# Kernel tuning notes

Hardware: AMD Instinct MI355X
Metric: run time of the kernel (lower is better)

Reference implementation:

```python
import jax, jax.numpy as jnp
import numpy as np

N, E = 10000, 320000
IN_CH, HID, OUT_CH, HEADS = 128, 64, 40, 8
NEG_SLOPE = 0.2


def gat_conv(x, src, dst, W, a_src, a_dst, bias, heads, C, concat, n_nodes):
    # x: [N, F_in]; W: [F_in, heads*C]; a_src/a_dst: [heads, C]
    h = (x @ W).reshape(n_nodes, heads, C)              # [N,H,C]
    alpha_src = jnp.sum(h * a_src, axis=-1)             # [N,H]
    alpha_dst = jnp.sum(h * a_dst, axis=-1)             # [N,H]
    score = jax.nn.leaky_relu(alpha_src[src] + alpha_dst[dst], NEG_SLOPE)  # [E,H]
    # segment softmax over edges sharing the same destination node
    smax = jax.ops.segment_max(score, dst, num_segments=n_nodes)
    smax = jnp.where(jnp.isfinite(smax), smax, 0.0)
    ex = jnp.exp(score - smax[dst])
    denom = jax.ops.segment_sum(ex, dst, num_segments=n_nodes)
    alpha = ex / (denom[dst] + 1e-16)                   # [E,H]
    msg = h[src] * alpha[:, :, None]                    # [E,H,C]
    out = jax.ops.segment_sum(msg, dst, num_segments=n_nodes)  # [N,H,C]
    out = out.reshape(n_nodes, heads * C) if concat else out.mean(axis=1)
    return out + bias


def setup_inputs() -> dict:
    key = jax.random.key(0)
    ks = jax.random.split(key, 16)
    g = 0.1
    return {
        "x": jax.random.normal(ks[0], (N, IN_CH), jnp.float32),
        "edge_index": jax.random.randint(ks[1], (2, E), 0, N, jnp.int64),
        "W1": jax.random.normal(ks[2], (IN_CH, HID), jnp.float32) * g,
        "b1": jnp.zeros((HID,), jnp.float32),
        "Wc1": jax.random.normal(ks[3], (HID, HEADS * HID), jnp.float32) * g,
        "att_src1": jax.random.normal(ks[4], (HEADS, HID), jnp.float32) * g,
        "att_dst1": jax.random.normal(ks[5], (HEADS, HID), jnp.float32) * g,
        "bc1": jnp.zeros((HEADS * HID,), jnp.float32),
        "Wc2": jax.random.normal(ks[6], (HEADS * HID, HID), jnp.float32) * g,
        "att_src2": jax.random.normal(ks[7], (1, HID), jnp.float32) * g,
        "att_dst2": jax.random.normal(ks[8], (1, HID), jnp.float32) * g,
        "bc2": jnp.zeros((HID,), jnp.float32),
        "W2": jax.random.normal(ks[9], (HID, OUT_CH), jnp.float32) * g,
        "b2": jnp.zeros((OUT_CH,), jnp.float32),
    }


def reference(x, edge_index, W1, b1, Wc1, att_src1, att_dst1, bc1,
              Wc2, att_src2, att_dst2, bc2, W2, b2):
    # add self-loops (PyG GATConv default add_self_loops=True)
    loop = jnp.arange(N, dtype=edge_index.dtype)
    src = jnp.concatenate([edge_index[0], loop])
    dst = jnp.concatenate([edge_index[1], loop])

    h = jax.nn.relu(x @ W1 + b1)                                   # lin0 + relu (dropout off in eval)
    h = jax.nn.elu(gat_conv(h, src, dst, Wc1, att_src1, att_dst1, bc1,
                            HEADS, HID, True, N))                  # conv1, concat heads
    h = gat_conv(h, src, dst, Wc2, att_src2, att_dst2, bc2,
                 1, HID, False, N)                                 # conv2, single head
    return h @ W2 + b2
```

## Files before the change

kernel.cpp:

```cpp
#include <hip/hip_runtime.h>
#include <cstdint>
#include <cstddef>

#define IN_CH 128
#define HID 64
#define HEADS 8
#define OUT_CH 40
#define NEG 0.2f
#define PAD 128

typedef __attribute__((ext_vector_type(8))) short bf16x8;
typedef __attribute__((ext_vector_type(4))) float f32x4;

#define MFMA(a, b, c) __builtin_amdgcn_mfma_f32_16x16x32_bf16(a, b, c, 0, 0, 0)

__device__ inline unsigned short f2bf(float f) {
    unsigned u = __float_as_uint(f);
    unsigned r = (u + 0x7FFFu + ((u >> 16) & 1u)) >> 16;
    return (unsigned short)r;
}
__device__ inline float bf2f(unsigned short b) {
    return __uint_as_float((unsigned)b << 16);
}
__device__ inline bf16x8 ldb8(const unsigned short* p) {
    return *reinterpret_cast<const bf16x8*>(p);
}


__global__ void k_init(const float* __restrict__ W1,
                       const float* __restrict__ Wc1, const float* __restrict__ Wc2,
                       const float* __restrict__ as1, const float* __restrict__ ad1,
                       int* __restrict__ cursor,
                       unsigned short* __restrict__ W1T,
                       unsigned short* __restrict__ Wc1T, unsigned short* __restrict__ Wc2T,
                       float* __restrict__ va_s, float* __restrict__ va_d, int N) {
    int i = blockIdx.x * 256 + threadIdx.x;
    if (i < N) { cursor[i] = 0; return; }
    i -= N;
    if (i < 64 * 128) {
        int j = i >> 7, k = i & 127;
        W1T[i] = f2bf(W1[k * 64 + j]);
        return;
    }
    i -= 64 * 128;
    if (i < 512 * 64) {
        int j = i >> 6, k = i & 63;
        Wc1T[i] = f2bf(Wc1[(size_t)k * 512 + j]);
        return;
    }
    i -= 512 * 64;
    if (i < 64 * 512) {
        int j = i >> 9, k = i & 511;
        Wc2T[i] = f2bf(Wc2[(size_t)k * 64 + j]);
        return;
    }
    i -= 64 * 512;
    if (i < 1024) {
        int sel = i >> 9, u = i & 511, j = u >> 3, h = u & 7;
        const float* a = sel ? ad1 : as1;
        float sum = 0.f;
        for (int c = 0; c < 64; ++c) sum += Wc1[(size_t)j * 512 + h * 64 + c] * a[h * 64 + c];
        (sel ? va_d : va_s)[j * 8 + h] = sum;
    }
}


__global__ void k_fillpad(const int* __restrict__ ei, int E, int N,
                          int* __restrict__ cursor, int* __restrict__ csrc) {
    int e = blockIdx.x * 256 + threadIdx.x;
    int T = E + N;
    if (e >= T) return;
    int s, d;
    if (e < E) { s = ei[e]; d = ei[E + e]; } else { s = d = e - E; }
    int pos = atomicAdd(&cursor[d], 1);
    csrc[(size_t)d * PAD + pos] = s;
}


__global__ __launch_bounds__(256) void k_lin1m(const float* __restrict__ x,
                                               const unsigned short* __restrict__ W1T,
                                               const float* __restrict__ b1,
                                               const float* __restrict__ va_s, const float* __restrict__ va_d,
                                               unsigned short* __restrict__ h0b,
                                               float* __restrict__ asrc, float* __restrict__ adst, int N) {
    __shared__ float pS[4][16][8], pD[4][16][8];
    int w = threadIdx.x >> 6, l = threadIdx.x & 63;
    int m0 = blockIdx.x * 16;
    int c = l & 15, g = l >> 4;
    bf16x8 af[4];
    const float* arow = x + (size_t)(m0 + c) * 128 + 8 * g;
#pragma unroll
    for (int ks = 0; ks < 4; ++ks) {
        float4 f0 = *(const float4*)(arow + 32 * ks);
        float4 f1 = *(const float4*)(arow + 32 * ks + 4);
        bf16x8 t;
        t[0] = (short)f2bf(f0.x); t[1] = (short)f2bf(f0.y);
        t[2] = (short)f2bf(f0.z); t[3] = (short)f2bf(f0.w);
        t[4] = (short)f2bf(f1.x); t[5] = (short)f2bf(f1.y);
        t[6] = (short)f2bf(f1.z); t[7] = (short)f2bf(f1.w);
        af[ks] = t;
    }
    f32x4 acc = {};
    const unsigned short* brow = W1T + (size_t)(16 * w + c) * 128 + 8 * g;
#pragma unroll
    for (int ks = 0; ks < 4; ++ks) acc = MFMA(af[ks], ldb8(brow + 32 * ks), acc);
    int j = 16 * w + c;
    float bj = b1[j];
    float4 vs0 = *(const float4*)&va_s[j * 8], vs1 = *(const float4*)&va_s[j * 8 + 4];
    float4 vd0 = *(const float4*)&va_d[j * 8], vd1 = *(const float4*)&va_d[j * 8 + 4];
#pragma unroll
    for (int r = 0; r < 4; ++r) {
        float v = fmaxf(acc[r] + bj, 0.f);
        h0b[(size_t)(m0 + 4 * g + r) * 64 + j] = f2bf(v);
        float s0 = v * vs0.x, s1 = v * vs0.y, s2 = v * vs0.z, s3 = v * vs0.w;
        float s4 = v * vs1.x, s5 = v * vs1.y, s6 = v * vs1.z, s7 = v * vs1.w;
        float d0 = v * vd0.x, d1 = v * vd0.y, d2 = v * vd0.z, d3 = v * vd0.w;
        float d4 = v * vd1.x, d5 = v * vd1.y, d6 = v * vd1.z, d7 = v * vd1.w;
#pragma unroll
        for (int off = 1; off < 16; off <<= 1) {
            s0 += __shfl_xor(s0, off); s1 += __shfl_xor(s1, off);
            s2 += __shfl_xor(s2, off); s3 += __shfl_xor(s3, off);
            s4 += __shfl_xor(s4, off); s5 += __shfl_xor(s5, off);
            s6 += __shfl_xor(s6, off); s7 += __shfl_xor(s7, off);
            d0 += __shfl_xor(d0, off); d1 += __shfl_xor(d1, off);
            d2 += __shfl_xor(d2, off); d3 += __shfl_xor(d3, off);
            d4 += __shfl_xor(d4, off); d5 += __shfl_xor(d5, off);
            d6 += __shfl_xor(d6, off); d7 += __shfl_xor(d7, off);
        }
        if (c == 0) {
            int row = 4 * g + r;
            pS[w][row][0] = s0; pS[w][row][1] = s1; pS[w][row][2] = s2; pS[w][row][3] = s3;
            pS[w][row][4] = s4; pS[w][row][5] = s5; pS[w][row][6] = s6; pS[w][row][7] = s7;
            pD[w][row][0] = d0; pD[w][row][1] = d1; pD[w][row][2] = d2; pD[w][row][3] = d3;
            pD[w][row][4] = d4; pD[w][row][5] = d5; pD[w][row][6] = d6; pD[w][row][7] = d7;
        }
    }
    __syncthreads();
    int tid = threadIdx.x;
    if (tid < 128) {
        int row = tid >> 3, h = tid & 7;
        float s = pS[0][row][h] + pS[1][row][h] + pS[2][row][h] + pS[3][row][h];
        float d = pD[0][row][h] + pD[1][row][h] + pD[2][row][h] + pD[3][row][h];
        int n = m0 + row;
        asrc[n * 8 + h] = s;
        adst[n * 8 + h] = d;
    }
}


__global__ __launch_bounds__(128) void k_conv1agg(const unsigned short* __restrict__ h0b,
                                                  const float* __restrict__ asrc, const float* __restrict__ adst,
                                                  const int* __restrict__ degs, const int* __restrict__ csrc,
                                                  unsigned short* __restrict__ aggb, int N) {
    __shared__ int srcb[PAD];
    __shared__ float sb[PAD][8];
    __shared__ float mx[8], den[8], adl[8];
    __shared__ float accsh[512];
    int tid = threadIdx.x;
    int n = blockIdx.x;
    int deg = degs[n];
    if (tid < 8) adl[tid] = adst[n * 8 + tid];
    __syncthreads();
    if (tid < deg) {
        int s = csrc[(size_t)n * PAD + tid];
        srcb[tid] = s;
        const float4* ap = (const float4*)&asrc[(size_t)s * 8];
        float4 a0 = ap[0], a1 = ap[1];
        float v;
        v = a0.x + adl[0]; sb[tid][0] = (v >= 0.f) ? v : NEG * v;
        v = a0.y + adl[1]; sb[tid][1] = (v >= 0.f) ? v : NEG * v;
        v = a0.z + adl[2]; sb[tid][2] = (v >= 0.f) ? v : NEG * v;
        v = a0.w + adl[3]; sb[tid][3] = (v >= 0.f) ? v : NEG * v;
        v = a1.x + adl[4]; sb[tid][4] = (v >= 0.f) ? v : NEG * v;
        v = a1.y + adl[5]; sb[tid][5] = (v >= 0.f) ? v : NEG * v;
        v = a1.z + adl[6]; sb[tid][6] = (v >= 0.f) ? v : NEG * v;
        v = a1.w + adl[7]; sb[tid][7] = (v >= 0.f) ? v : NEG * v;
    }
    __syncthreads();
    if (tid < 64) {
        int hh = tid & 7, idx = tid >> 3;
        float m = -1e30f;
        for (int i = idx; i < deg; i += 8) m = fmaxf(m, sb[i][hh]);
        m = fmaxf(m, __shfl_xor(m, 8));
        m = fmaxf(m, __shfl_xor(m, 16));
        m = fmaxf(m, __shfl_xor(m, 32));
        if (tid < 8) mx[tid] = m;
    }
    __syncthreads();
    for (int idx = tid; idx < deg * 8; idx += 128) {
        int i = idx >> 3, hh = idx & 7;
        sb[i][hh] = __expf(sb[i][hh] - mx[hh]);
    }
    __syncthreads();
    if (tid < 64) {
        int hh = tid & 7, idx = tid >> 3;
        float d = 0.f;
        for (int i = idx; i < deg; i += 8) d += sb[i][hh];
        d += __shfl_xor(d, 8);
        d += __shfl_xor(d, 16);
        d += __shfl_xor(d, 32);
        if (tid < 8) den[tid] = d + 1e-16f;
    }
    int lane = tid & 63, wv = tid >> 6;
    int half = lane >> 5, cl = lane & 31;
    float accA[8] = {0.f, 0.f, 0.f, 0.f, 0.f, 0.f, 0.f, 0.f};
    float accB[8] = {0.f, 0.f, 0.f, 0.f, 0.f, 0.f, 0.f, 0.f};
    for (int i = 2 * wv; i < deg; i += 4) {
        int e = i + half;
        float vx = 0.f, vy = 0.f;
        float4 w0 = {0.f, 0.f, 0.f, 0.f}, w1 = {0.f, 0.f, 0.f, 0.f};
        if (e < deg) {
            unsigned u = *(const unsigned*)&h0b[(size_t)srcb[e] * 64 + 2 * cl];
            vx = bf2f((unsigned short)(u & 0xFFFFu));
            vy = bf2f((unsigned short)(u >> 16));
            w0 = *(const float4*)&sb[e][0];
            w1 = *(const float4*)&sb[e][4];
        }
        accA[0] += w0.x * vx; accB[0] += w0.x * vy;
        accA[1] += w0.y * vx; accB[1] += w0.y * vy;
        accA[2] += w0.z * vx; accB[2] += w0.z * vy;
        accA[3] += w0.w * vx; accB[3] += w0.w * vy;
        accA[4] += w1.x * vx; accB[4] += w1.x * vy;
        accA[5] += w1.y * vx; accB[5] += w1.y * vy;
        accA[6] += w1.z * vx; accB[6] += w1.z * vy;
        accA[7] += w1.w * vx; accB[7] += w1.w * vy;
    }
#pragma unroll
    for (int h = 0; h < 8; ++h) {
        accA[h] += __shfl_xor(accA[h], 32);
        accB[h] += __shfl_xor(accB[h], 32);
    }
    __syncthreads();
    if (wv == 1 && half == 0) {
#pragma unroll
        for (int h = 0; h < 8; ++h) {
            accsh[h * 64 + 2 * cl] = accA[h];
            accsh[h * 64 + 2 * cl + 1] = accB[h];
        }
    }
    __syncthreads();
    if (wv == 0 && half == 0) {
#pragma unroll
        for (int h = 0; h < 8; ++h) {
            float t0 = (accA[h] + accsh[h * 64 + 2 * cl]) / den[h];
            float t1 = (accB[h] + accsh[h * 64 + 2 * cl + 1]) / den[h];
            unsigned uo = (unsigned)f2bf(t0) | ((unsigned)f2bf(t1) << 16);
            *(unsigned*)&aggb[(size_t)n * 512 + h * 64 + 2 * cl] = uo;
        }
    }
}


__global__ __launch_bounds__(512) void k_p1l2(const unsigned short* __restrict__ aggb,
                                              const unsigned short* __restrict__ Wc1T,
                                              const float* __restrict__ bc1,
                                              const unsigned short* __restrict__ Wc2T,
                                              const float* __restrict__ as2, const float* __restrict__ ad2,
                                              unsigned short* __restrict__ hc2b,
                                              float* __restrict__ asrc, float* __restrict__ adst, int N) {
    __shared__ unsigned short h1s[16][520];
    __shared__ float part[7][4][64][4];
    int w = threadIdx.x >> 6, l = threadIdx.x & 63;
    int m0 = blockIdx.x * 16;
    int c = l & 15, g = l >> 4;
    {
        const unsigned short* arow = aggb + (size_t)(m0 + c) * 512 + w * 64 + 8 * g;
        bf16x8 af0 = ldb8(arow), af1 = ldb8(arow + 32);
        f32x4 acc[4] = {};
#pragma unroll
        for (int nt = 0; nt < 4; ++nt) {
            const unsigned short* brow = Wc1T + (size_t)(w * 64 + 16 * nt + c) * 64 + 8 * g;
            acc[nt] = MFMA(af0, ldb8(brow), acc[nt]);
            acc[nt] = MFMA(af1, ldb8(brow + 32), acc[nt]);
        }
#pragma unroll
        for (int nt = 0; nt < 4; ++nt) {
            int j = w * 64 + 16 * nt + c;
            float bj = bc1[j];
#pragma unroll
            for (int r = 0; r < 4; ++r) {
                float v = acc[nt][r] + bj;
                v = (v > 0.f) ? v : __expf(v) - 1.f;
                h1s[4 * g + r][j] = f2bf(v);
            }
        }
    }
    __syncthreads();
    f32x4 acc2[4] = {};
#pragma unroll
    for (int ks = 0; ks < 2; ++ks) {
        bf16x8 af = ldb8(&h1s[c][64 * w + 32 * ks + 8 * g]);
#pragma unroll
        for (int nt = 0; nt < 4; ++nt) {
            const unsigned short* brow = Wc2T + (size_t)(16 * nt + c) * 512 + 64 * w + 32 * ks + 8 * g;
            acc2[nt] = MFMA(af, ldb8(brow), acc2[nt]);
        }
    }
    if (w > 0) {
#pragma unroll
        for (int nt = 0; nt < 4; ++nt)
            *(f32x4*)&part[w - 1][nt][l][0] = acc2[nt];
    }
    __syncthreads();
    if (w != 0) return;
#pragma unroll
    for (int nt = 0; nt < 4; ++nt)
#pragma unroll
        for (int i = 0; i < 7; ++i) {
            f32x4 pp = *(const f32x4*)&part[i][nt][l][0];
            acc2[nt][0] += pp[0]; acc2[nt][1] += pp[1];
            acc2[nt][2] += pp[2]; acc2[nt][3] += pp[3];
        }
    float ps[4] = {0.f, 0.f, 0.f, 0.f}, pd[4] = {0.f, 0.f, 0.f, 0.f};
#pragma unroll
    for (int nt = 0; nt < 4; ++nt) {
        int j = 16 * nt + c;
        float aj = as2[j], dj = ad2[j];
#pragma unroll
        for (int r = 0; r < 4; ++r) {
            float v = acc2[nt][r];
            hc2b[(size_t)(m0 + 4 * g + r) * 64 + j] = f2bf(v);
            ps[r] += v * aj;
            pd[r] += v * dj;
        }
    }
#pragma unroll
    for (int r = 0; r < 4; ++r) {
        float s = ps[r], d = pd[r];
        s += __shfl_xor(s, 1); s += __shfl_xor(s, 2); s += __shfl_xor(s, 4); s += __shfl_xor(s, 8);
        d += __shfl_xor(d, 1); d += __shfl_xor(d, 2); d += __shfl_xor(d, 4); d += __shfl_xor(d, 8);
        if (c == 0) {
            int n = m0 + 4 * g + r;
            asrc[n] = s;
            adst[n] = d;
        }
    }
}


__global__ __launch_bounds__(256) void k_conv2f(const unsigned short* __restrict__ hc2b,
                                                const float* __restrict__ asrc, const float* __restrict__ adst,
                                                const int* __restrict__ degs, const int* __restrict__ csrc,
                                                const float* __restrict__ bc2,
                                                const float* __restrict__ W2, const float* __restrict__ b2,
                                                float* __restrict__ out, int N) {
    __shared__ float w2s[HID * OUT_CH];
    __shared__ float cosh_[4][HID];
    int tid = threadIdx.x;
    for (int i = tid; i < HID * OUT_CH; i += 256) w2s[i] = W2[i];
    int lane = tid & 63, nl = tid >> 6;
    int half = lane >> 5, cl = lane & 31;
    int n = blockIdx.x * 4 + nl;
    if (n < N) {
        int deg = degs[n];
        float ad = adst[n];
        float rm = -1e30f, rden = 0.f;
        float ax = 0.f, ay = 0.f;
        for (int base = 0; base < deg; base += 64) {
            int cnt = min(64, deg - base);
            int s = 0;
            float sc = -1e30f;
            if (lane < cnt) {
                s = csrc[(size_t)n * PAD + base + lane];
                float v = asrc[s] + ad;
                sc = (v >= 0.f) ? v : NEG * v;
            }
            float m = sc;
#pragma unroll
            for (int mm = 1; mm < 64; mm <<= 1) m = fmaxf(m, __shfl_xor(m, mm));
            float nmv = fmaxf(rm, m);
            float scale = __expf(rm - nmv);
            float p = (lane < cnt) ? __expf(sc - nmv) : 0.f;
            float d = p;
#pragma unroll
            for (int mm = 1; mm < 64; mm <<= 1) d += __shfl_xor(d, mm);
            rden = rden * scale + d;
            rm = nmv;
            ax *= scale; ay *= scale;
            for (int i = 0; i < cnt; i += 2) {
                int idx = i + half;
                float pi = __shfl(p, idx);
                int si = __shfl(s, idx);
                unsigned u = *(const unsigned*)&hc2b[(size_t)si * 64 + 2 * cl];
                ax += pi * bf2f((unsigned short)(u & 0xFFFFu));
                ay += pi * bf2f((unsigned short)(u >> 16));
            }
        }
        ax += __shfl_xor(ax, 32);
        ay += __shfl_xor(ay, 32);
        if (half == 0) {
            float inv = 1.f / (rden + 1e-16f);
            cosh_[nl][2 * cl] = ax * inv + bc2[2 * cl];
            cosh_[nl][2 * cl + 1] = ay * inv + bc2[2 * cl + 1];
        }
    }
    __syncthreads();
    if (tid >= 160) return;
    int nn = tid / 40, j = tid % 40;
    int no = blockIdx.x * 4 + nn;
    if (no >= N) return;
    float s = b2[j];
#pragma unroll 8
    for (int k = 0; k < HID; ++k) s += cosh_[nn][k] * w2s[k * OUT_CH + j];
    out[(size_t)no * OUT_CH + j] = s;
}


extern "C" void kernel_launch(void* const* d_in, const int* in_sizes, int n_in,
                              void* d_out, int out_size, void* d_ws, size_t ws_size,
                              hipStream_t stream) {
    const float* x   = (const float*)d_in[0];
    const int*   ei  = (const int*)d_in[1];
    const float* W1  = (const float*)d_in[2];
    const float* b1  = (const float*)d_in[3];
    const float* Wc1 = (const float*)d_in[4];
    const float* as1 = (const float*)d_in[5];
    const float* ad1 = (const float*)d_in[6];
    const float* bc1 = (const float*)d_in[7];
    const float* Wc2 = (const float*)d_in[8];
    const float* as2 = (const float*)d_in[9];
    const float* ad2 = (const float*)d_in[10];
    const float* bc2 = (const float*)d_in[11];
    const float* W2  = (const float*)d_in[12];
    const float* b2  = (const float*)d_in[13];

    const int N = in_sizes[0] / IN_CH;
    const int E = in_sizes[1] / 2;
    const int T = E + N;

    char* base = (char*)d_ws;
    size_t off = 0;
    auto carve = [&](size_t bytes) -> void* {
        off = (off + 255) & ~(size_t)255;
        void* r = base + off;
        off += bytes;
        return r;
    };
    int* cursor     = (int*)carve((size_t)N * 4);
    int* csrc       = (int*)carve((size_t)N * PAD * 4);
    unsigned short* W1T  = (unsigned short*)carve((size_t)64 * 128 * 2);
    unsigned short* Wc1T = (unsigned short*)carve((size_t)512 * 64 * 2);
    unsigned short* Wc2T = (unsigned short*)carve((size_t)64 * 512 * 2);
    float* va_s     = (float*)carve((size_t)512 * 4);
    float* va_d     = (float*)carve((size_t)512 * 4);
    unsigned short* h0b  = (unsigned short*)carve((size_t)N * 64 * 2);
    float* asrc1    = (float*)carve((size_t)N * 8 * 4);
    float* adst1    = (float*)carve((size_t)N * 8 * 4);
    unsigned short* aggb = (unsigned short*)carve((size_t)N * 512 * 2);
    unsigned short* hc2b = (unsigned short*)carve((size_t)N * 64 * 2);
    float* asrc2    = (float*)carve((size_t)N * 4);
    float* adst2    = (float*)carve((size_t)N * 4);

    int init_total = N + 64 * 128 + 512 * 64 + 64 * 512 + 1024;
    k_init<<<(init_total + 255) / 256, 256, 0, stream>>>(W1, Wc1, Wc2, as1, ad1, cursor,
                                                         W1T, Wc1T, Wc2T, va_s, va_d, N);
    k_fillpad<<<(T + 255) / 256, 256, 0, stream>>>(ei, E, N, cursor, csrc);

    k_lin1m<<<(N + 15) / 16, 256, 0, stream>>>(x, W1T, b1, va_s, va_d, h0b, asrc1, adst1, N);
    k_conv1agg<<<N, 128, 0, stream>>>(h0b, asrc1, adst1, cursor, csrc, aggb, N);
    k_p1l2<<<(N + 15) / 16, 512, 0, stream>>>(aggb, Wc1T, bc1, Wc2T, as2, ad2,
                                              hc2b, asrc2, adst2, N);
    k_conv2f<<<(N + 3) / 4, 256, 0, stream>>>(hc2b, asrc2, adst2, cursor, csrc, bc2, W2, b2,
                                              (float*)d_out, N);
}
```

Measured before the change: 109.8 us.

## Fuse CSR fill into lin1 kernel and compute attention logits via MFMA

Merges the edge-bucketing fill kernel into the first linear kernel as extra blocks, removing one launch and letting the two independent workloads overlap. The per-node attention logits are now produced by a small MFMA over a bf16 transposed attention-weight matrix staged through shared memory, replacing the 16-way shuffle reductions. The softmax exp pass is merged into the denominator loop, removing one sync and one pass over shared memory. The bf16 logit weights add rounding error, and the fused kernel mixes two unrelated block roles.

Result: faster. 96.56 us (-12.1%).

```diff
diff --git a/kernel.cpp b/kernel.cpp
--- a/kernel.cpp
+++ b/kernel.cpp
@@ -33,7 +33,7 @@
                        int* __restrict__ cursor,
                        unsigned short* __restrict__ W1T,
                        unsigned short* __restrict__ Wc1T, unsigned short* __restrict__ Wc2T,
-                       float* __restrict__ va_s, float* __restrict__ va_d, int N) {
+                       unsigned short* __restrict__ vaT, int N) {
     int i = blockIdx.x * 256 + threadIdx.x;
     if (i < N) { cursor[i] = 0; return; }
     i -= N;
@@ -56,39 +56,42 @@
     }
     i -= 64 * 512;
     if (i < 1024) {
-        int sel = i >> 9, u = i & 511, j = u >> 3, h = u & 7;
-        const float* a = sel ? ad1 : as1;
+        int t = i >> 6, k = i & 63;
+        int h = t & 7;
+        const float* a = (t < 8) ? as1 : ad1;
         float sum = 0.f;
-        for (int c = 0; c < 64; ++c) sum += Wc1[(size_t)j * 512 + h * 64 + c] * a[h * 64 + c];
-        (sel ? va_d : va_s)[j * 8 + h] = sum;
-    }
-}
-
-
-__global__ void k_fillpad(const int* __restrict__ ei, int E, int N,
-                          int* __restrict__ cursor, int* __restrict__ csrc) {
-    int e = blockIdx.x * 256 + threadIdx.x;
-    int T = E + N;
-    if (e >= T) return;
-    int s, d;
-    if (e < E) { s = ei[e]; d = ei[E + e]; } else { s = d = e - E; }
-    int pos = atomicAdd(&cursor[d], 1);
-    csrc[(size_t)d * PAD + pos] = s;
+        for (int c = 0; c < 64; ++c) sum += Wc1[(size_t)k * 512 + h * 64 + c] * a[h * 64 + c];
+        vaT[t * 64 + k] = f2bf(sum);
+    }
 }
 
 
 __global__ __launch_bounds__(256) void k_lin1m(const float* __restrict__ x,
                                                const unsigned short* __restrict__ W1T,
                                                const float* __restrict__ b1,
-                                               const float* __restrict__ va_s, const float* __restrict__ va_d,
+                                               const unsigned short* __restrict__ vaT,
                                                unsigned short* __restrict__ h0b,
-                                               float* __restrict__ asrc, float* __restrict__ adst, int N) {
-    __shared__ float pS[4][16][8], pD[4][16][8];
+                                               float* __restrict__ asrc, float* __restrict__ adst,
+                                               const int* __restrict__ ei, int E, int T,
+                                               int* __restrict__ cursor, int* __restrict__ csrc,
+                                               int N, int NB) {
+    __shared__ unsigned short h0s[16][72];
+    if (blockIdx.x >= NB) {
+        int e = (blockIdx.x - NB) * 256 + threadIdx.x;
+        if (e < T) {
+            int s, d;
+            if (e < E) { s = ei[e]; d = ei[E + e]; } else { s = d = e - E; }
+            int pos = atomicAdd(&cursor[d], 1);
+            csrc[(size_t)d * PAD + pos] = s;
+        }
+        return;
+    }
     int w = threadIdx.x >> 6, l = threadIdx.x & 63;
     int m0 = blockIdx.x * 16;
     int c = l & 15, g = l >> 4;
+    int xr = m0 + c; if (xr >= N) xr = N - 1;
     bf16x8 af[4];
-    const float* arow = x + (size_t)(m0 + c) * 128 + 8 * g;
+    const float* arow = x + (size_t)xr * 128 + 8 * g;
 #pragma unroll
     for (int ks = 0; ks < 4; ++ks) {
         float4 f0 = *(const float4*)(arow + 32 * ks);
@@ -106,44 +109,31 @@
     for (int ks = 0; ks < 4; ++ks) acc = MFMA(af[ks], ldb8(brow + 32 * ks), acc);
     int j = 16 * w + c;
     float bj = b1[j];
-    float4 vs0 = *(const float4*)&va_s[j * 8], vs1 = *(const float4*)&va_s[j * 8 + 4];
-    float4 vd0 = *(const float4*)&va_d[j * 8], vd1 = *(const float4*)&va_d[j * 8 + 4];
 #pragma unroll
     for (int r = 0; r < 4; ++r) {
         float v = fmaxf(acc[r] + bj, 0.f);
-        h0b[(size_t)(m0 + 4 * g + r) * 64 + j] = f2bf(v);
-        float s0 = v * vs0.x, s1 = v * vs0.y, s2 = v * vs0.z, s3 = v * vs0.w;
-        float s4 = v * vs1.x, s5 = v * vs1.y, s6 = v * vs1.z, s7 = v * vs1.w;
-        float d0 = v * vd0.x, d1 = v * vd0.y, d2 = v * vd0.z, d3 = v * vd0.w;
-        float d4 = v * vd1.x, d5 = v * vd1.y, d6 = v * vd1.z, d7 = v * vd1.w;
-#pragma unroll
-        for (int off = 1; off < 16; off <<= 1) {
-            s0 += __shfl_xor(s0, off); s1 += __shfl_xor(s1, off);
-            s2 += __shfl_xor(s2, off); s3 += __shfl_xor(s3, off);
-            s4 += __shfl_xor(s4, off); s5 += __shfl_xor(s5, off);
-            s6 += __shfl_xor(s6, off); s7 += __shfl_xor(s7, off);
-            d0 += __shfl_xor(d0, off); d1 += __shfl_xor(d1, off);
-            d2 += __shfl_xor(d2, off); d3 += __shfl_xor(d3, off);
-            d4 += __shfl_xor(d4, off); d5 += __shfl_xor(d5, off);
-            d6 += __shfl_xor(d6, off); d7 += __shfl_xor(d7, off);
-        }
-        if (c == 0) {
-            int row = 4 * g + r;
-            pS[w][row][0] = s0; pS[w][row][1] = s1; pS[w][row][2] = s2; pS[w][row][3] = s3;
-            pS[w][row][4] = s4; pS[w][row][5] = s5; pS[w][row][6] = s6; pS[w][row][7] = s7;
-            pD[w][row][0] = d0; pD[w][row][1] = d1; pD[w][row][2] = d2; pD[w][row][3] = d3;
-            pD[w][row][4] = d4; pD[w][row][5] = d5; pD[w][row][6] = d6; pD[w][row][7] = d7;
-        }
-    }
-    __syncthreads();
-    int tid = threadIdx.x;
-    if (tid < 128) {
-        int row = tid >> 3, h = tid & 7;
-        float s = pS[0][row][h] + pS[1][row][h] + pS[2][row][h] + pS[3][row][h];
-        float d = pD[0][row][h] + pD[1][row][h] + pD[2][row][h] + pD[3][row][h];
-        int n = m0 + row;
-        asrc[n * 8 + h] = s;
-        adst[n * 8 + h] = d;
+        unsigned short us = f2bf(v);
+        int row = m0 + 4 * g + r;
+        if (row < N) h0b[(size_t)row * 64 + j] = us;
+        h0s[4 * g + r][j] = us;
+    }
+    __syncthreads();
+    if (w == 0) {
+        bf16x8 a0 = ldb8(&h0s[c][8 * g]);
+        bf16x8 a1 = ldb8(&h0s[c][32 + 8 * g]);
+        bf16x8 b0 = ldb8(&vaT[c * 64 + 8 * g]);
+        bf16x8 b1v = ldb8(&vaT[c * 64 + 32 + 8 * g]);
+        f32x4 al = {};
+        al = MFMA(a0, b0, al);
+        al = MFMA(a1, b1v, al);
+#pragma unroll
+        for (int r = 0; r < 4; ++r) {
+            int n = m0 + 4 * g + r;
+            if (n < N) {
+                if (c < 8) asrc[n * 8 + c] = al[r];
+                else       adst[n * 8 + (c - 8)] = al[r];
+            }
+        }
     }
 }
 
@@ -187,20 +177,21 @@
         if (tid < 8) mx[tid] = m;
     }
     __syncthreads();
-    for (int idx = tid; idx < deg * 8; idx += 128) {
-        int i = idx >> 3, hh = idx & 7;
-        sb[i][hh] = __expf(sb[i][hh] - mx[hh]);
-    }
-    __syncthreads();
     if (tid < 64) {
         int hh = tid & 7, idx = tid >> 3;
+        float mh = mx[hh];
         float d = 0.f;
-        for (int i = idx; i < deg; i += 8) d += sb[i][hh];
+        for (int i = idx; i < deg; i += 8) {
+            float e = __expf(sb[i][hh] - mh);
+            sb[i][hh] = e;
+            d += e;
+        }
         d += __shfl_xor(d, 8);
         d += __shfl_xor(d, 16);
         d += __shfl_xor(d, 32);
         if (tid < 8) den[tid] = d + 1e-16f;
     }
+    __syncthreads();
     int lane = tid & 63, wv = tid >> 6;
     int half = lane >> 5, cl = lane & 31;
     float accA[8] = {0.f, 0.f, 0.f, 0.f, 0.f, 0.f, 0.f, 0.f};
@@ -441,8 +432,7 @@
     unsigned short* W1T  = (unsigned short*)carve((size_t)64 * 128 * 2);
     unsigned short* Wc1T = (unsigned short*)carve((size_t)512 * 64 * 2);
     unsigned short* Wc2T = (unsigned short*)carve((size_t)64 * 512 * 2);
-    float* va_s     = (float*)carve((size_t)512 * 4);
-    float* va_d     = (float*)carve((size_t)512 * 4);
+    unsigned short* vaT  = (unsigned short*)carve((size_t)16 * 64 * 2);
     unsigned short* h0b  = (unsigned short*)carve((size_t)N * 64 * 2);
     float* asrc1    = (float*)carve((size_t)N * 8 * 4);
     float* adst1    = (float*)carve((size_t)N * 8 * 4);
@@ -453,10 +443,12 @@
 
     int init_total = N + 64 * 128 + 512 * 64 + 64 * 512 + 1024;
     k_init<<<(init_total + 255) / 256, 256, 0, stream>>>(W1, Wc1, Wc2, as1, ad1, cursor,
-                                                         W1T, Wc1T, Wc2T, va_s, va_d, N);
-    k_fillpad<<<(T + 255) / 256, 256, 0, stream>>>(ei, E, N, cursor, csrc);
-
-    k_lin1m<<<(N + 15) / 16, 256, 0, stream>>>(x, W1T, b1, va_s, va_d, h0b, asrc1, adst1, N);
+                                                         W1T, Wc1T, Wc2T, vaT, N);
+
+    int NB = (N + 15) / 16;
+    int FB = (T + 255) / 256;
+    k_lin1m<<<NB + FB, 256, 0, stream>>>(x, W1T, b1, vaT, h0b, asrc1, adst1,
+                                         ei, E, T, cursor, csrc, N, NB);
     k_conv1agg<<<N, 128, 0, stream>>>(h0b, asrc1, adst1, cursor, csrc, aggb, N);
     k_p1l2<<<(N + 15) / 16, 512, 0, stream>>>(aggb, Wc1T, bc1, Wc2T, as2, ad2,
                                               hc2b, asrc2, adst2, N);
```
